# Performance work log

Measured on AMD Instinct MI355X. Metric: run time of the kernel, lower is better.

## Reference

```python
import jax, jax.numpy as jnp
import numpy as np

N, IN_C, HEADS, OUT_C = 4096, 256, 4, 64
NEG_SLOPE = 0.2


def setup_inputs() -> dict:
    key = jax.random.key(0)
    k1, k2, k3, k4, k5 = jax.random.split(key, 5)
    x = jax.random.normal(k1, (N, IN_C), dtype=jnp.float32)
    adj = jax.random.randint(k2, (N, N), 0, 2, dtype=jnp.int32)
    # xavier-uniform style scales
    s_w = float(np.sqrt(6.0 / (IN_C + HEADS * OUT_C)))
    s_a = float(np.sqrt(6.0 / (HEADS + OUT_C)))
    W = jax.random.uniform(k3, (IN_C, HEADS * OUT_C), jnp.float32, -s_w, s_w)
    att_l = jax.random.uniform(k4, (HEADS, OUT_C), jnp.float32, -s_a, s_a)
    att_r = jax.random.uniform(k5, (HEADS, OUT_C), jnp.float32, -s_a, s_a)
    bias = jnp.zeros((HEADS * OUT_C,), jnp.float32)
    return {"x": x, "adj": adj, "W": W, "att_l": att_l, "att_r": att_r, "bias": bias}


def reference(x, adj, W, att_l, att_r, bias):
    n = x.shape[0]
    h = (x @ W).reshape(n, HEADS, OUT_C)              # [N, H, C]
    el = jnp.einsum('nhc,hc->nh', h, att_l)           # [N, H]
    er = jnp.einsum('nhc,hc->nh', h, att_r)           # [N, H]
    e = el[:, None, :] + er[None, :, :]               # [N, N, H]
    e = jnp.where(e >= 0, e, NEG_SLOPE * e)           # leaky_relu
    mask = (adj > 0)[:, :, None]                      # [N, N, 1]
    e = jnp.where(mask, e, -jnp.inf)
    alpha = jax.nn.softmax(e, axis=1)                 # softmax over j
    out = jnp.einsum('ijh,jhc->ihc', alpha, h)        # [N, H, C]
    out = out.reshape(n, HEADS * OUT_C) + bias
    return out
```

## Files before the change

### kernel.cpp

```cpp
#include <hip/hip_runtime.h>
#include <hip/hip_bf16.h>
#include <stdint.h>

typedef float f32x4 __attribute__((ext_vector_type(4)));
typedef short s16x8 __attribute__((ext_vector_type(8)));
typedef int   i32x4 __attribute__((ext_vector_type(4)));
typedef _Float16 f16x4 __attribute__((ext_vector_type(4)));
typedef unsigned int u32;

#define NNODES 4096
#define NEG    0.2f
#define SJ     8
#define JL     512
#define OUTF   256

__device__ __forceinline__ unsigned short f2bf(float f) {
  unsigned u = __float_as_uint(f);
  u += 0x7FFFu + ((u >> 16) & 1u);
  return (unsigned short)(u >> 16);
}
__device__ __forceinline__ unsigned encf(float x) {
  unsigned u = __float_as_uint(x);
  return (u & 0x80000000u) ? ~u : (u | 0x80000000u);
}
__device__ __forceinline__ float decf(unsigned e) {
  unsigned u = (e & 0x80000000u) ? (e ^ 0x80000000u) : ~e;
  return __uint_as_float(u);
}

__global__ __launch_bounds__(256) void k_prep(
    const float* __restrict__ W, const float* __restrict__ attl,
    const float* __restrict__ attr,
    unsigned short* __restrict__ WT, float* __restrict__ Wlr)
{
  __shared__ float wt[8 * 256];
  __shared__ float att_s[512];
  const int tid = threadIdx.x;
  const int kr = tid >> 5, l32 = tid & 31;
  const int k = blockIdx.x * 8 + kr;
  const float* wrow = W + (size_t)k * 256 + l32 * 8;
  f32x4 w0 = *(const f32x4*)(wrow);
  f32x4 w1 = *(const f32x4*)(wrow + 4);
  *(f32x4*)(wt + kr * 256 + l32 * 8)     = w0;
  *(f32x4*)(wt + kr * 256 + l32 * 8 + 4) = w1;
  att_s[tid]       = attl[tid];
  att_s[256 + tid] = attr[tid];
  __syncthreads();

  float pl = 0.f, pr = 0.f;
#pragma unroll
  for (int i = 0; i < 4; ++i) {
    pl += w0[i] * att_s[l32 * 8 + i] + w1[i] * att_s[l32 * 8 + 4 + i];
    pr += w0[i] * att_s[256 + l32 * 8 + i] + w1[i] * att_s[256 + l32 * 8 + 4 + i];
  }
  pl += __shfl_xor(pl, 1, 64); pl += __shfl_xor(pl, 2, 64); pl += __shfl_xor(pl, 4, 64);
  pr += __shfl_xor(pr, 1, 64); pr += __shfl_xor(pr, 2, 64); pr += __shfl_xor(pr, 4, 64);
  if ((l32 & 7) == 0) {
    Wlr[k * 8 + (l32 >> 3)]     = pl;
    Wlr[k * 8 + 4 + (l32 >> 3)] = pr;
  }
  {
    const int c = tid;
    unsigned v[4];
#pragma unroll
    for (int i = 0; i < 4; ++i) {
      unsigned lo = f2bf(wt[(2 * i) * 256 + c]);
      unsigned hi = f2bf(wt[(2 * i + 1) * 256 + c]);
      v[i] = lo | (hi << 16);
    }
    const int gW = blockIdx.x;
    const int pos = (gW & 24) | ((gW & 7) ^ (c & 7));
    *(uint4*)(WT + (size_t)c * 256 + pos * 8) = make_uint4(v[0], v[1], v[2], v[3]);
  }
}

__global__ __launch_bounds__(256) void k_el(
    const float* __restrict__ x, const float* __restrict__ Wlr,
    float* __restrict__ el_t, u32* __restrict__ QS,
    unsigned* __restrict__ M_enc, unsigned short* __restrict__ xbf)
{
  __shared__ float wls[16 * 145];
  __shared__ float er_s[64];
  const int tid = threadIdx.x;
  {
    f32x4 a = *(const f32x4*)(Wlr + tid * 8);
    f32x4 b = *(const f32x4*)(Wlr + tid * 8 + 4);
    float* d = wls + (tid >> 4) * 145 + (tid & 15) * 9;
    *(f32x4*)d = a; *(f32x4*)(d + 4) = b;
  }
  __syncthreads();
  const int nl = tid >> 4, l15 = tid & 15;
  const int n = blockIdx.x * 16 + nl;
  f32x4 xv[4];
#pragma unroll
  for (int i = 0; i < 4; ++i)
    xv[i] = *(const f32x4*)(x + (size_t)n * 256 + l15 * 16 + i * 4);
  f32x4 al = {0.f,0.f,0.f,0.f}, ar = {0.f,0.f,0.f,0.f};
  const float* wb = wls + l15 * 145;
#pragma unroll
  for (int i = 0; i < 16; ++i) {
    float xi = xv[i >> 2][i & 3];
    f32x4 wl = *(const f32x4*)(wb + i * 9);
    f32x4 wr = *(const f32x4*)(wb + i * 9 + 4);
    al += xi * wl; ar += xi * wr;
  }
#pragma unroll
  for (int m = 1; m < 16; m <<= 1)
#pragma unroll
    for (int c = 0; c < 4; ++c) {
      al[c] += __shfl_xor(al[c], m, 64);
      ar[c] += __shfl_xor(ar[c], m, 64);
    }
  if (l15 == 0) {
#pragma unroll
    for (int h = 0; h < 4; ++h) {
      el_t[h * NNODES + n] = al[h];
      float q = __expf(ar[h]);
      float s = __expf(NEG * ar[h]);
      QS[h * NNODES + n] = (u32)f2bf(q) | ((u32)f2bf(s) << 16);
      er_s[nl * 4 + h] = ar[h];
    }
  }
  {
    u32 pk[8];
#pragma unroll
    for (int i = 0; i < 8; ++i) {
      unsigned lo = f2bf(xv[(2 * i) >> 2][(2 * i) & 3]);
      unsigned hi = f2bf(xv[(2 * i + 1) >> 2][(2 * i + 1) & 3]);
      pk[i] = lo | (hi << 16);
    }
    const int key = n & 7;
    const int g0 = l15 * 2;
    const int p0 = (g0 & 24) | ((g0 & 7) ^ key);
    const int p1 = (g0 & 24) | (((g0 + 1) & 7) ^ key);
    unsigned short* xb = xbf + (size_t)n * 256;
    *(uint4*)(xb + p0 * 8) = make_uint4(pk[0], pk[1], pk[2], pk[3]);
    *(uint4*)(xb + p1 * 8) = make_uint4(pk[4], pk[5], pk[6], pk[7]);
  }
  __syncthreads();
  if (tid < 64) {
    float v = er_s[tid];
    v = fmaxf(v, __shfl_xor(v, 4, 64));
    v = fmaxf(v, __shfl_xor(v, 8, 64));
    v = fmaxf(v, __shfl_xor(v, 16, 64));
    v = fmaxf(v, __shfl_xor(v, 32, 64));
    if (tid < 4) atomicMax(M_enc + tid, encf(v));
  }
}

__global__ __launch_bounds__(256) void k_hmm(
    const unsigned short* __restrict__ xbf, const unsigned short* __restrict__ WT,
    unsigned short* __restrict__ hT)
{
  __shared__ __align__(16) unsigned short xs[128 * 256];
  __shared__ __align__(16) unsigned short ws[64 * 256];
  const int tid = threadIdx.x, wv = tid >> 6, lane = tid & 63;
  const int l15 = lane & 15, lg = lane >> 4;
  const int c0 = blockIdx.x * 64, n0 = blockIdx.y * 128;
#pragma unroll
  for (int q = 0; q < 16; ++q) {
    const int r2 = (wv * 16 + q) * 2;
    __builtin_amdgcn_global_load_lds(
        xbf + (size_t)(n0 + r2 + (lane >> 5)) * 256 + (lane & 31) * 8,
        xs + r2 * 256, 16, 0, 0);
  }
#pragma unroll
  for (int q = 0; q < 8; ++q) {
    const int r2 = (wv * 8 + q) * 2;
    __builtin_amdgcn_global_load_lds(
        WT + (size_t)(c0 + r2 + (lane >> 5)) * 256 + (lane & 31) * 8,
        ws + r2 * 256, 16, 0, 0);
  }
  __syncthreads();
  f32x4 acc[8];
#pragma unroll
  for (int nt = 0; nt < 8; ++nt) acc[nt] = (f32x4){0.f,0.f,0.f,0.f};
  const int key = l15 & 7;
#pragma unroll
  for (int kk = 0; kk < 8; ++kk) {
    const int G = kk * 4 + lg;
    const int pos = (G & 24) | ((G & 7) ^ key);
    s16x8 a = *(const s16x8*)(ws + (wv * 16 + l15) * 256 + pos * 8);
#pragma unroll
    for (int nt = 0; nt < 8; ++nt) {
      s16x8 b = *(const s16x8*)(xs + (nt * 16 + l15) * 256 + pos * 8);
      acc[nt] = __builtin_amdgcn_mfma_f32_16x16x32_bf16(a, b, acc[nt], 0, 0, 0);
    }
  }
#pragma unroll
  for (int nt = 0; nt < 8; ++nt)
#pragma unroll
    for (int r = 0; r < 4; ++r) {
      const int c = c0 + wv * 16 + lg * 4 + r;
      const int nloc = nt * 16 + l15;
      const int gl = nloc >> 3;
      const int posn = (gl & 8) | ((gl & 7) ^ (c & 7));
      hT[(size_t)c * NNODES + n0 + posn * 8 + (nloc & 7)] = f2bf(acc[nt][r]);
    }
}

__global__ __launch_bounds__(512, 2) void k_gat(
    const int* __restrict__ adj, const unsigned short* __restrict__ hT,
    const float* __restrict__ el_t, const u32* __restrict__ QS,
    const unsigned* __restrict__ M_enc,
    _Float16* __restrict__ nump, float* __restrict__ denp)
{
  __shared__ __align__(16) unsigned short hbuf[256 * 256];
  __shared__ __align__(16) u32 qsb[4 * JL];

  const int tid = threadIdx.x;
  const int wid = tid >> 6, lane = tid & 63;
  const int l15 = lane & 15, lg = lane >> 4;
  const int i0 = blockIdx.x * 128 + wid * 16;
  const int js = blockIdx.y;
  const int j0 = js * JL;
  const int key = l15 & 7;

  float P[4], R[4];
#pragma unroll
  for (int h = 0; h < 4; ++h) {
    float el  = el_t[h * NNODES + i0 + l15];
    float M   = decf(M_enc[h]);
    float sE  = el + M;
    float mih = fmaxf(sE, NEG * sE);
    P[h] = __expf(el - mih);
    R[h] = __expf(NEG * el - mih);
  }

  __builtin_amdgcn_global_load_lds(
      QS + (size_t)(wid >> 1) * NNODES + j0 + (wid & 1) * 256 + lane * 4,
      qsb + (wid >> 1) * JL + (wid & 1) * 256, 16, 0, 0);

  const int* asrc = adj + (size_t)(i0 + l15) * NNODES + j0 + lg * 8;

  f32x4 acc[4][4];
  f32x4 accd[4];
#pragma unroll
  for (int h = 0; h < 4; ++h) {
    accd[h] = (f32x4){0.f, 0.f, 0.f, 0.f};
#pragma unroll
    for (int c = 0; c < 4; ++c) acc[h][c] = (f32x4){0.f, 0.f, 0.f, 0.f};
  }
  s16x8 ones;
#pragma unroll
  for (int e = 0; e < 8; ++e) ones[e] = (short)0x3F80;

#define STAGE(p)                                                                 \
  do {                                                                           \
    _Pragma("unroll")                                                            \
    for (int q = 0; q < 16; ++q) {                                               \
      const int c2 = wid * 32 + q * 2;                                           \
      __builtin_amdgcn_global_load_lds(                                          \
          hT + (size_t)(c2 + (lane >> 5)) * NNODES + j0 + (p) * 256 + (lane & 31) * 8, \
          hbuf + c2 * 256, 16, 0, 0);                                            \
    }                                                                            \
  } while (0)

  STAGE(0);

#pragma unroll
  for (int p = 0; p < 2; ++p) {
    if (p == 1) {
      __syncthreads();
      STAGE(1);
    }
    i32x4 a0 = *(const i32x4*)(asrc + p * 256);
    i32x4 a1 = *(const i32x4*)(asrc + p * 256 + 4);
    __syncthreads();

#pragma unroll
    for (int K = 0; K < 8; ++K) {
      const int nK = (K < 7) ? (K + 1) : 7;
      i32x4 na0 = *(const i32x4*)(asrc + p * 256 + nK * 32);
      i32x4 na1 = *(const i32x4*)(asrc + p * 256 + nK * 32 + 4);

      const int pos = (K >> 1) * 64 + ((((K & 1) * 4 + lg) ^ key) * 8);

#pragma unroll
      for (int h = 0; h < 4; ++h) {
        const unsigned short* lb = hbuf + (h * 64 + l15) * 256 + pos;
        s16x8 b0 = *(const s16x8*)(lb);
        s16x8 b1 = *(const s16x8*)(lb + 16 * 256);
        s16x8 b2 = *(const s16x8*)(lb + 32 * 256);
        s16x8 b3 = *(const s16x8*)(lb + 48 * 256);
        const u32* qrow = qsb + h * JL + p * 256 + K * 32 + lg * 8;
        i32x4 q0 = *(const i32x4*)(qrow);
        i32x4 q1 = *(const i32x4*)(qrow + 4);

        float w[8];
#pragma unroll
        for (int e = 0; e < 4; ++e) {
          u32 m0 = (a0[e] > 0) ? (u32)q0[e] : 0u;
          u32 m1 = (a1[e] > 0) ? (u32)q1[e] : 0u;
          float qq0 = __uint_as_float(m0 << 16);
          float ss0 = __uint_as_float(m0 & 0xffff0000u);
          float qq1 = __uint_as_float(m1 << 16);
          float ss1 = __uint_as_float(m1 & 0xffff0000u);
          w[e]     = fmaxf(P[h] * qq0, R[h] * ss0);
          w[e + 4] = fmaxf(P[h] * qq1, R[h] * ss1);
        }
        union { u32 uu[4]; s16x8 v; } af;
#pragma unroll
        for (int pp = 0; pp < 4; ++pp)
          asm("v_cvt_pk_bf16_f32 %0, %1, %2"
              : "=v"(af.uu[pp]) : "v"(w[2 * pp]), "v"(w[2 * pp + 1]));

        acc[h][0] = __builtin_amdgcn_mfma_f32_16x16x32_bf16(af.v, b0,   acc[h][0], 0, 0, 0);
        acc[h][1] = __builtin_amdgcn_mfma_f32_16x16x32_bf16(af.v, b1,   acc[h][1], 0, 0, 0);
        acc[h][2] = __builtin_amdgcn_mfma_f32_16x16x32_bf16(af.v, b2,   acc[h][2], 0, 0, 0);
        acc[h][3] = __builtin_amdgcn_mfma_f32_16x16x32_bf16(af.v, b3,   acc[h][3], 0, 0, 0);
        accd[h]   = __builtin_amdgcn_mfma_f32_16x16x32_bf16(af.v, ones, accd[h],   0, 0, 0);
      }
      a0 = na0; a1 = na1;
    }
  }
#undef STAGE

  const int orow = i0 + lg * 4;
#pragma unroll
  for (int h = 0; h < 4; ++h) {
    _Float16* np = nump + ((size_t)js * NNODES + orow) * OUTF + h * 64 + l15;
#pragma unroll
    for (int c = 0; c < 4; ++c)
#pragma unroll
      for (int r = 0; r < 4; ++r)
        np[r * OUTF + c * 16] = (_Float16)acc[h][c][r];
  }
  if (l15 == 0) {
    float* dp = denp + ((size_t)js * NNODES + orow) * 4;
#pragma unroll
    for (int h = 0; h < 4; ++h)
#pragma unroll
      for (int r = 0; r < 4; ++r) dp[r * 4 + h] = accd[h][r];
  }
}

__global__ __launch_bounds__(256) void k_div(
    const _Float16* __restrict__ nump, const float* __restrict__ denp,
    const float* __restrict__ bias, float* __restrict__ out)
{
  const int q  = blockIdx.x * 256 + threadIdx.x;
  const int n  = q >> 6;
  const int c4 = (q & 63) * 4;
  const int h  = c4 >> 6;
  f32x4 s = {0.f, 0.f, 0.f, 0.f};
  float d = 0.f;
#pragma unroll
  for (int t = 0; t < SJ; ++t) {
    f16x4 v = *(const f16x4*)(nump + ((size_t)t * NNODES + n) * OUTF + c4);
    s[0] += (float)v[0]; s[1] += (float)v[1];
    s[2] += (float)v[2]; s[3] += (float)v[3];
    d += denp[((size_t)t * NNODES + n) * 4 + h];
  }
  f32x4 b = *(const f32x4*)(bias + c4);
  float r = __builtin_amdgcn_rcpf(d);
  f32x4 o = s * r + b;
  *(f32x4*)(out + (size_t)n * OUTF + c4) = o;
}

extern "C" void kernel_launch(void* const* d_in, const int* in_sizes, int n_in,
                              void* d_out, int out_size, void* d_ws, size_t ws_size,
                              hipStream_t stream)
{
  const float* x    = (const float*)d_in[0];
  const int*   adj  = (const int*)d_in[1];
  const float* W    = (const float*)d_in[2];
  const float* attl = (const float*)d_in[3];
  const float* attr = (const float*)d_in[4];
  const float* bias = (const float*)d_in[5];
  float* out = (float*)d_out;
  char*  ws  = (char*)d_ws;

  unsigned short* hT   = (unsigned short*)ws;
  float*     el_t  = (float*)(ws + (2u << 20));
  u32*       QS    = (u32*)(ws + (2u << 20) + (64u << 10));
  unsigned*  M_enc = (unsigned*)(ws + (2u << 20) + (128u << 10));
  float*     denp  = (float*)(ws + (2u << 20) + (192u << 10));
  unsigned short* WT = (unsigned short*)(ws + (2u << 20) + (704u << 10));
  float*     Wlr   = (float*)(ws + (2u << 20) + (832u << 10));
  _Float16*  nump  = (_Float16*)(ws + (3u << 20));
  unsigned short* xbf = (unsigned short*)(ws + (17u << 20));

  hipMemsetAsync(M_enc, 0, 16, stream);
  k_prep<<<32, 256, 0, stream>>>(W, attl, attr, WT, Wlr);
  k_el<<<256, 256, 0, stream>>>(x, Wlr, el_t, QS, M_enc, xbf);
  k_hmm<<<dim3(4, 32), 256, 0, stream>>>(xbf, WT, hT);
  k_gat<<<dim3(32, SJ), 512, 0, stream>>>(adj, hT, el_t, QS, M_enc, nump, denp);
  k_div<<<1024, 256, 0, stream>>>(nump, denp, bias, out);
}
```

Baseline: 62.49 us.

## Split heads across waves and halve LDS tile to raise k_gat occupancy

Each block now covers 64 rows instead of 128. Its 8 waves are split into 4 row-chunks times 2 head-groups, so each wave accumulates only 2 heads. This halves the accumulator registers, and the hT staging tile shrinks to 128 columns across 4 phases, which halves LDS use and allows 3 blocks per CU and twice as many blocks. The cost is that adjacency rows are read twice, once per head-group wave, and there are more barriers per j-slice.

```diff
diff --git a/kernel.cpp b/kernel.cpp
--- a/kernel.cpp
+++ b/kernel.cpp
@@ -199,47 +199,50 @@
     }
 }
 
-__global__ __launch_bounds__(512, 2) void k_gat(
+__global__ __launch_bounds__(512, 3) void k_gat(
     const int* __restrict__ adj, const unsigned short* __restrict__ hT,
     const float* __restrict__ el_t, const u32* __restrict__ QS,
     const unsigned* __restrict__ M_enc,
     _Float16* __restrict__ nump, float* __restrict__ denp)
 {
-  __shared__ __align__(16) unsigned short hbuf[256 * 256];
+  __shared__ __align__(16) unsigned short hbuf[256 * 128];
   __shared__ __align__(16) u32 qsb[4 * JL];
 
   const int tid = threadIdx.x;
   const int wid = tid >> 6, lane = tid & 63;
   const int l15 = lane & 15, lg = lane >> 4;
-  const int i0 = blockIdx.x * 128 + wid * 16;
+  const int ic = wid & 3, hg = wid >> 2;
+  const int i0 = blockIdx.x * 64;
   const int js = blockIdx.y;
   const int j0 = js * JL;
+  const int irow = i0 + ic * 16 + l15;
   const int key = l15 & 7;
 
-  float P[4], R[4];
-#pragma unroll
-  for (int h = 0; h < 4; ++h) {
-    float el  = el_t[h * NNODES + i0 + l15];
+  float P[2], R[2];
+#pragma unroll
+  for (int hh = 0; hh < 2; ++hh) {
+    const int h = hg * 2 + hh;
+    float el  = el_t[h * NNODES + irow];
     float M   = decf(M_enc[h]);
     float sE  = el + M;
     float mih = fmaxf(sE, NEG * sE);
-    P[h] = __expf(el - mih);
-    R[h] = __expf(NEG * el - mih);
+    P[hh] = __expf(el - mih);
+    R[hh] = __expf(NEG * el - mih);
   }
 
   __builtin_amdgcn_global_load_lds(
       QS + (size_t)(wid >> 1) * NNODES + j0 + (wid & 1) * 256 + lane * 4,
       qsb + (wid >> 1) * JL + (wid & 1) * 256, 16, 0, 0);
 
-  const int* asrc = adj + (size_t)(i0 + l15) * NNODES + j0 + lg * 8;
-
-  f32x4 acc[4][4];
-  f32x4 accd[4];
-#pragma unroll
-  for (int h = 0; h < 4; ++h) {
-    accd[h] = (f32x4){0.f, 0.f, 0.f, 0.f};
-#pragma unroll
-    for (int c = 0; c < 4; ++c) acc[h][c] = (f32x4){0.f, 0.f, 0.f, 0.f};
+  const int* asrc = adj + (size_t)irow * NNODES + j0 + lg * 8;
+
+  f32x4 acc[2][4];
+  f32x4 accd[2];
+#pragma unroll
+  for (int hh = 0; hh < 2; ++hh) {
+    accd[hh] = (f32x4){0.f, 0.f, 0.f, 0.f};
+#pragma unroll
+    for (int c = 0; c < 4; ++c) acc[hh][c] = (f32x4){0.f, 0.f, 0.f, 0.f};
   }
   s16x8 ones;
 #pragma unroll
@@ -248,42 +251,45 @@
 #define STAGE(p)                                                                 \
   do {                                                                           \
     _Pragma("unroll")                                                            \
-    for (int q = 0; q < 16; ++q) {                                               \
-      const int c2 = wid * 32 + q * 2;                                           \
+    for (int q = 0; q < 8; ++q) {                                                \
+      const int r4 = (wid * 8 + q) * 4;                                          \
       __builtin_amdgcn_global_load_lds(                                          \
-          hT + (size_t)(c2 + (lane >> 5)) * NNODES + j0 + (p) * 256 + (lane & 31) * 8, \
-          hbuf + c2 * 256, 16, 0, 0);                                            \
+          hT + (size_t)(r4 + (lane >> 4)) * NNODES + j0 + (p) * 128 + (lane & 15) * 8, \
+          hbuf + r4 * 128, 16, 0, 0);                                            \
     }                                                                            \
   } while (0)
 
   STAGE(0);
-
-#pragma unroll
-  for (int p = 0; p < 2; ++p) {
-    if (p == 1) {
+  i32x4 a0 = *(const i32x4*)(asrc);
+  i32x4 a1 = *(const i32x4*)(asrc + 4);
+
+#pragma unroll
+  for (int p = 0; p < 4; ++p) {
+    if (p) {
       __syncthreads();
-      STAGE(1);
-    }
-    i32x4 a0 = *(const i32x4*)(asrc + p * 256);
-    i32x4 a1 = *(const i32x4*)(asrc + p * 256 + 4);
+      STAGE(p);
+    }
     __syncthreads();
 
 #pragma unroll
-    for (int K = 0; K < 8; ++K) {
-      const int nK = (K < 7) ? (K + 1) : 7;
-      i32x4 na0 = *(const i32x4*)(asrc + p * 256 + nK * 32);
-      i32x4 na1 = *(const i32x4*)(asrc + p * 256 + nK * 32 + 4);
-
-      const int pos = (K >> 1) * 64 + ((((K & 1) * 4 + lg) ^ key) * 8);
-
-#pragma unroll
-      for (int h = 0; h < 4; ++h) {
-        const unsigned short* lb = hbuf + (h * 64 + l15) * 256 + pos;
+    for (int K = 0; K < 4; ++K) {
+      const int t = p * 4 + K;
+      const int tn = (t < 15) ? t + 1 : t;
+      i32x4 na0 = *(const i32x4*)(asrc + tn * 32);
+      i32x4 na1 = *(const i32x4*)(asrc + tn * 32 + 4);
+
+      const int G0 = K * 4 + lg;
+      const int pos = (G0 & 8) | ((G0 & 7) ^ key);
+
+#pragma unroll
+      for (int hh = 0; hh < 2; ++hh) {
+        const int h = hg * 2 + hh;
+        const unsigned short* lb = hbuf + (h * 64 + l15) * 128 + pos * 8;
         s16x8 b0 = *(const s16x8*)(lb);
-        s16x8 b1 = *(const s16x8*)(lb + 16 * 256);
-        s16x8 b2 = *(const s16x8*)(lb + 32 * 256);
-        s16x8 b3 = *(const s16x8*)(lb + 48 * 256);
-        const u32* qrow = qsb + h * JL + p * 256 + K * 32 + lg * 8;
+        s16x8 b1 = *(const s16x8*)(lb + 16 * 128);
+        s16x8 b2 = *(const s16x8*)(lb + 32 * 128);
+        s16x8 b3 = *(const s16x8*)(lb + 48 * 128);
+        const u32* qrow = qsb + h * JL + t * 32 + lg * 8;
         i32x4 q0 = *(const i32x4*)(qrow);
         i32x4 q1 = *(const i32x4*)(qrow + 4);
 
@@ -296,8 +302,8 @@
           float ss0 = __uint_as_float(m0 & 0xffff0000u);
           float qq1 = __uint_as_float(m1 << 16);
           float ss1 = __uint_as_float(m1 & 0xffff0000u);
-          w[e]     = fmaxf(P[h] * qq0, R[h] * ss0);
-          w[e + 4] = fmaxf(P[h] * qq1, R[h] * ss1);
+          w[e]     = fmaxf(P[hh] * qq0, R[hh] * ss0);
+          w[e + 4] = fmaxf(P[hh] * qq1, R[hh] * ss1);
         }
         union { u32 uu[4]; s16x8 v; } af;
 #pragma unroll
@@ -305,33 +311,34 @@
           asm("v_cvt_pk_bf16_f32 %0, %1, %2"
               : "=v"(af.uu[pp]) : "v"(w[2 * pp]), "v"(w[2 * pp + 1]));
 
-        acc[h][0] = __builtin_amdgcn_mfma_f32_16x16x32_bf16(af.v, b0,   acc[h][0], 0, 0, 0);
-        acc[h][1] = __builtin_amdgcn_mfma_f32_16x16x32_bf16(af.v, b1,   acc[h][1], 0, 0, 0);
-        acc[h][2] = __builtin_amdgcn_mfma_f32_16x16x32_bf16(af.v, b2,   acc[h][2], 0, 0, 0);
-        acc[h][3] = __builtin_amdgcn_mfma_f32_16x16x32_bf16(af.v, b3,   acc[h][3], 0, 0, 0);
-        accd[h]   = __builtin_amdgcn_mfma_f32_16x16x32_bf16(af.v, ones, accd[h],   0, 0, 0);
+        acc[hh][0] = __builtin_amdgcn_mfma_f32_16x16x32_bf16(af.v, b0,   acc[hh][0], 0, 0, 0);
+        acc[hh][1] = __builtin_amdgcn_mfma_f32_16x16x32_bf16(af.v, b1,   acc[hh][1], 0, 0, 0);
+        acc[hh][2] = __builtin_amdgcn_mfma_f32_16x16x32_bf16(af.v, b2,   acc[hh][2], 0, 0, 0);
+        acc[hh][3] = __builtin_amdgcn_mfma_f32_16x16x32_bf16(af.v, b3,   acc[hh][3], 0, 0, 0);
+        accd[hh]   = __builtin_amdgcn_mfma_f32_16x16x32_bf16(af.v, ones, accd[hh],   0, 0, 0);
       }
       a0 = na0; a1 = na1;
     }
   }
 #undef STAGE
 
-  const int orow = i0 + lg * 4;
-#pragma unroll
-  for (int h = 0; h < 4; ++h) {
+  const int orow = i0 + ic * 16 + lg * 4;
+#pragma unroll
+  for (int hh = 0; hh < 2; ++hh) {
+    const int h = hg * 2 + hh;
     _Float16* np = nump + ((size_t)js * NNODES + orow) * OUTF + h * 64 + l15;
 #pragma unroll
     for (int c = 0; c < 4; ++c)
 #pragma unroll
       for (int r = 0; r < 4; ++r)
-        np[r * OUTF + c * 16] = (_Float16)acc[h][c][r];
+        np[r * OUTF + c * 16] = (_Float16)acc[hh][c][r];
   }
   if (l15 == 0) {
     float* dp = denp + ((size_t)js * NNODES + orow) * 4;
 #pragma unroll
-    for (int h = 0; h < 4; ++h)
-#pragma unroll
-      for (int r = 0; r < 4; ++r) dp[r * 4 + h] = accd[h][r];
+    for (int hh = 0; hh < 2; ++hh)
+#pragma unroll
+      for (int r = 0; r < 4; ++r) dp[r * 4 + hg * 2 + hh] = accd[hh][r];
   }
 }
 
@@ -385,6 +392,6 @@
   k_prep<<<32, 256, 0, stream>>>(W, attl, attr, WT, Wlr);
   k_el<<<256, 256, 0, stream>>>(x, Wlr, el_t, QS, M_enc, xbf);
   k_hmm<<<dim3(4, 32), 256, 0, stream>>>(xbf, WT, hT);
-  k_gat<<<dim3(32, SJ), 512, 0, stream>>>(adj, hT, el_t, QS, M_enc, nump, denp);
+  k_gat<<<dim3(64, SJ), 512, 0, stream>>>(adj, hT, el_t, QS, M_enc, nump, denp);
   k_div<<<1024, 256, 0, stream>>>(nump, denp, bias, out);
 }
```

Result: no change. 62.15 us, median of 2 (-0.5%).
